# Kernel tuning notes

Hardware: AMD Instinct MI355X
Metric: run time of the kernel (lower is better)

## Reference

```python
import jax, jax.numpy as jnp
import numpy as np

N, LMAX, D, VOCAB, CVOCAB = 50000, 12, 512, 1552, 80


def setup_inputs() -> dict:
    key = jax.random.key(0)
    ks = jax.random.split(key, 8)
    return {
        "word_ids": jax.random.randint(ks[0], (N,), 0, VOCAB),
        "char_ids": jax.random.randint(ks[1], (N, LMAX), 0, CVOCAB),
        "char_lens": jax.random.randint(ks[2], (N,), 1, LMAX + 1),
        "word_embed_table": jax.random.normal(ks[3], (VOCAB, D), jnp.float32) * 0.02,
        "char_embed_table": jax.random.normal(ks[4], (CVOCAB, D), jnp.float32) * 0.02,
        "char_proj_w": jax.random.normal(ks[5], (D,), jnp.float32) * 0.04,
        "char_proj_b": jnp.zeros((1,), jnp.float32),
        "word_proj_w": jax.random.normal(ks[6], (D,), jnp.float32) * 0.04,
        "word_proj_b": jnp.zeros((1,), jnp.float32),
        "clf_w": jax.random.normal(ks[7], (VOCAB, D), jnp.float32) * 0.04,
        "clf_b": jnp.zeros((VOCAB,), jnp.float32),
    }


def reference(word_ids, char_ids, char_lens, word_embed_table, char_embed_table,
              char_proj_w, char_proj_b, word_proj_w, word_proj_b, clf_w, clf_b):
    # word embedding lookup: [N, D]
    we = word_embed_table[word_ids]
    # char embedding lookup (padded): [N, L, D]
    ce = char_embed_table[char_ids]
    # char_proj = Linear(512, 1): scores per char, [N, L]
    pre = jnp.einsum("nld,d->nl", ce, char_proj_w) + char_proj_b
    # mask out padding (reproduces the ragged per-word loop of the original)
    mask = (jnp.arange(LMAX) < char_lens[:, None]).astype(pre.dtype)  # [N, L]
    # attn_weights = pre_attn^T @ word_char_embed per word -> [N, D]
    char_pool = jnp.einsum("nl,nld->nd", pre * mask, ce)
    # all_embed = sigmoid(word_embed * char_embed): [N, D]
    all_embed = jax.nn.sigmoid(we * char_pool)
    # word_proj = Linear(512, 1) + Swish(beta=1): [N]
    wa = jnp.einsum("nd,d->n", all_embed, word_proj_w) + word_proj_b
    wa = wa * jax.nn.sigmoid(wa)
    # word_weights = word_attn^T @ all_embed: [1, D]
    word_weights = jnp.einsum("n,nd->d", wa, all_embed)[None, :]
    # classifier Linear(512, 1552): [1, VOCAB]
    res = word_weights @ clf_w.T + clf_b
    return (all_embed, res)
```

## Files before the change

kernel.cpp:

```cpp
#include <hip/hip_runtime.h>
#include <math.h>

#define LMAXC 12
#define DIM   512
#define VOC   1552
#define NCHAR 80

typedef float vf4 __attribute__((ext_vector_type(4)));
typedef _Float16 hf8 __attribute__((ext_vector_type(8)));
typedef unsigned short ushort_t;

#define WW8_OFF 0
#define U_OFF   4096
#define WT_OFF  25600

__device__ __forceinline__ float sigmoidf_fast(float x) {
    return 1.0f / (1.0f + __expf(-x));
}

__device__ __forceinline__ ushort_t f2bf(float f) {
    unsigned u = __float_as_uint(f);
    u = (u + 0x7fffu + ((u >> 16) & 1u)) >> 16;
    return (ushort_t)u;
}

__global__ __launch_bounds__(256)
void setup_kernel(const float* __restrict__ ctab,
                  const float* __restrict__ cpw,
                  const float* __restrict__ cpb,
                  const float* __restrict__ wtab,
                  float*       __restrict__ ws)
{
    __shared__ float red[4];
    const int b   = blockIdx.x;
    const int tid = threadIdx.x;
    _Float16* uh = (_Float16*)(ws + U_OFF);

    if (b < NCHAR) {
        const float a0 = ctab[b * DIM + tid];
        const float a1 = ctab[b * DIM + tid + 256];
        float p = a0 * cpw[tid] + a1 * cpw[tid + 256];
        #pragma unroll
        for (int off = 32; off > 0; off >>= 1) p += __shfl_xor(p, off, 64);
        if ((tid & 63) == 0) red[tid >> 6] = p;
        __syncthreads();
        const float s = red[0] + red[1] + red[2] + red[3] + cpb[0];
        uh[b * DIM + tid]       = (_Float16)(s * a0);
        uh[b * DIM + tid + 256] = (_Float16)(s * a1);
    } else if (b == NCHAR) {
        for (int i = tid; i < 8 * DIM; i += 256) ws[WW8_OFF + i] = 0.f;
        uh[NCHAR * DIM + tid]       = (_Float16)0.f;
        uh[NCHAR * DIM + tid + 256] = (_Float16)0.f;
    } else {
        const int r0 = (b - NCHAR - 1) * 4;
        ushort_t* wt16 = (ushort_t*)(ws + WT_OFF);
        #pragma unroll
        for (int i = 0; i < 8; ++i) {
            const int idx = r0 * DIM + i * 256 + tid;
            wt16[idx] = f2bf(wtab[idx]);
        }
    }
}

__device__ __forceinline__ void bf8_unpack(uint4 v, float* f) {
    f[0] = __uint_as_float(v.x << 16); f[1] = __uint_as_float(v.x & 0xffff0000u);
    f[2] = __uint_as_float(v.y << 16); f[3] = __uint_as_float(v.y & 0xffff0000u);
    f[4] = __uint_as_float(v.z << 16); f[5] = __uint_as_float(v.z & 0xffff0000u);
    f[6] = __uint_as_float(v.w << 16); f[7] = __uint_as_float(v.w & 0xffff0000u);
}

__global__ __launch_bounds__(256)
void fused_word_kernel(const int*   __restrict__ word_ids,
                       const int*   __restrict__ char_ids,
                       const int*   __restrict__ char_lens,
                       const float* __restrict__ wpw,
                       const float* __restrict__ wpb,
                       const float* __restrict__ ws,
                       float*       __restrict__ all_embed,
                       float*       __restrict__ ww8,
                       int n)
{
    const int lane = threadIdx.x & 63;
    const int wv   = threadIdx.x >> 6;
    const int d0   = lane << 3;
    const _Float16* uh   = (const _Float16*)(ws + U_OFF);
    const ushort_t* wt16 = (const ushort_t*)(ws + WT_OFF);

    const vf4 pw0 = *(const vf4*)(wpw + d0);
    const vf4 pw1 = *(const vf4*)(wpw + d0 + 4);
    const float wb = wpb[0];

    vf4 acc0 = {0.f, 0.f, 0.f, 0.f};
    vf4 acc1 = {0.f, 0.f, 0.f, 0.f};

    const int gw0     = (blockIdx.x << 2) + wv;
    const int gstride = gridDim.x << 2;

    int wu = 0, wid = 0, len = 0;
    int4 ci0 = {0,0,0,0}, ci1 = ci0, ci2 = ci0;

    int w = gw0;
    if (w < n) {
        wu  = __builtin_amdgcn_readfirstlane(w);
        wid = word_ids[wu];
        len = char_lens[wu];
        const int4* cp = (const int4*)(char_ids + (size_t)wu * LMAXC);
        ci0 = cp[0]; ci1 = cp[1]; ci2 = cp[2];
    }

    while (w < n) {
        const int wn  = w + gstride;
        const int wun = __builtin_amdgcn_readfirstlane(wn < n ? wn : 0);
        const int widn = word_ids[wun];
        const int lenn = char_lens[wun];
        const int4* cpn = (const int4*)(char_ids + (size_t)wun * LMAXC);
        const int4 m0 = cpn[0], m1 = cpn[1], m2 = cpn[2];

        const uint4 wvec = *(const uint4*)(wt16 + (size_t)wid * DIM + d0);

        const int cid[LMAXC] = {ci0.x, ci0.y, ci0.z, ci0.w,
                                ci1.x, ci1.y, ci1.z, ci1.w,
                                ci2.x, ci2.y, ci2.z, ci2.w};
        int cide[LMAXC];
        #pragma unroll
        for (int l = 0; l < LMAXC; ++l) cide[l] = (l < len) ? cid[l] : NCHAR;

        hf8 hsA = (hf8)(_Float16)0.f;
        hf8 hsB = (hf8)(_Float16)0.f;
        #pragma unroll
        for (int l = 0; l < LMAXC; l += 2) {
            const hf8 rA = *(const hf8*)(uh + cide[l]     * DIM + d0);
            const hf8 rB = *(const hf8*)(uh + cide[l + 1] * DIM + d0);
            hsA += rA;
            hsB += rB;
        }
        const hf8 hs = hsA + hsB;

        float p[8];
        #pragma unroll
        for (int j = 0; j < 8; ++j) p[j] = (float)hs[j];

        float we[8];
        bf8_unpack(wvec, we);
        float ae[8];
        #pragma unroll
        for (int j = 0; j < 8; ++j) ae[j] = sigmoidf_fast(we[j] * p[j]);

        const vf4 a0v = {ae[0], ae[1], ae[2], ae[3]};
        const vf4 a1v = {ae[4], ae[5], ae[6], ae[7]};

        float* op = all_embed + (size_t)wu * DIM + d0;
        __builtin_nontemporal_store(a0v, (vf4*)op);
        __builtin_nontemporal_store(a1v, (vf4*)(op + 4));

        float s = ae[0]*pw0.x + ae[1]*pw0.y + ae[2]*pw0.z + ae[3]*pw0.w
                + ae[4]*pw1.x + ae[5]*pw1.y + ae[6]*pw1.z + ae[7]*pw1.w;
        #pragma unroll
        for (int off = 32; off > 0; off >>= 1)
            s += __shfl_xor(s, off, 64);
        float wa = s + wb;
        wa = wa * sigmoidf_fast(wa);

        acc0 += wa * a0v;
        acc1 += wa * a1v;

        w = wn; wu = wun; wid = widn; len = lenn;
        ci0 = m0; ci1 = m1; ci2 = m2;
    }

    __shared__ float lds[4][DIM];
    *(vf4*)&lds[wv][d0]     = acc0;
    *(vf4*)&lds[wv][d0 + 4] = acc1;
    __syncthreads();

    const int slice = blockIdx.x & 7;
    for (int d = threadIdx.x; d < DIM; d += 256) {
        const float s = lds[0][d] + lds[1][d] + lds[2][d] + lds[3][d];
        atomicAdd(ww8 + slice * DIM + d, s);
    }
}

__global__ __launch_bounds__(256)
void clf_kernel(const float* __restrict__ ww8,
                const float* __restrict__ clf_w,
                const float* __restrict__ clf_b,
                float*       __restrict__ res)
{
    const int lane = threadIdx.x & 63;
    const int wv   = threadIdx.x >> 6;
    const int v    = (blockIdx.x << 2) + wv;
    if (v >= VOC) return;

    const int d0 = lane << 3;
    float w[8];
    #pragma unroll
    for (int j = 0; j < 8; ++j) w[j] = 0.f;
    #pragma unroll
    for (int s = 0; s < 8; ++s) {
        const float4 a = *(const float4*)(ww8 + s * DIM + d0);
        const float4 b = *(const float4*)(ww8 + s * DIM + d0 + 4);
        w[0] += a.x; w[1] += a.y; w[2] += a.z; w[3] += a.w;
        w[4] += b.x; w[5] += b.y; w[6] += b.z; w[7] += b.w;
    }

    const float* cr = clf_w + (size_t)v * DIM + d0;
    const float4 a0 = *(const float4*)(cr);
    const float4 a1 = *(const float4*)(cr + 4);
    float p = w[0]*a0.x + w[1]*a0.y + w[2]*a0.z + w[3]*a0.w
            + w[4]*a1.x + w[5]*a1.y + w[6]*a1.z + w[7]*a1.w;
    #pragma unroll
    for (int off = 32; off > 0; off >>= 1)
        p += __shfl_xor(p, off, 64);
    if (lane == 0) res[v] = p + clf_b[v];
}

extern "C" void kernel_launch(void* const* d_in, const int* in_sizes, int n_in,
                              void* d_out, int out_size, void* d_ws, size_t ws_size,
                              hipStream_t stream) {
    const int*   word_ids  = (const int*)  d_in[0];
    const int*   char_ids  = (const int*)  d_in[1];
    const int*   char_lens = (const int*)  d_in[2];
    const float* wtab      = (const float*)d_in[3];
    const float* ctab      = (const float*)d_in[4];
    const float* cpw       = (const float*)d_in[5];
    const float* cpb       = (const float*)d_in[6];
    const float* wpw       = (const float*)d_in[7];
    const float* wpb       = (const float*)d_in[8];
    const float* clf_w     = (const float*)d_in[9];
    const float* clf_b     = (const float*)d_in[10];

    const int n = in_sizes[0];
    float* out       = (float*)d_out;
    float* all_embed = out;
    float* res       = out + (size_t)n * DIM;
    float* ws        = (float*)d_ws;

    setup_kernel<<<NCHAR + 1 + (VOC / 4), 256, 0, stream>>>(ctab, cpw, cpb, wtab, ws);

    fused_word_kernel<<<2048, 256, 0, stream>>>(
        word_ids, char_ids, char_lens,
        wpw, wpb, ws, all_embed, ws + WW8_OFF, n);

    clf_kernel<<<(VOC + 3) / 4, 256, 0, stream>>>(ws + WW8_OFF, clf_w, clf_b, res);
}
```

Before: 47.08 us.

## Store scaled char table as FP8, stage it in LDS, prefetch word rows

The precomputed scaled char-embedding table is stored as FP8 with a power-of-two scale, which the word table absorbs as an inverse scale. Each block copies the whole table (about 41 KB) into LDS, so the gathers read shared memory instead of global or L2. The word-table row for the next word is now prefetched one iteration ahead, and blocks grow to 512 threads with half as many blocks. FP8 quantisation lowers accuracy of the char pooling, and the per-block LDS fill plus higher LDS use may reduce occupancy.

```diff
diff --git a/kernel.cpp b/kernel.cpp
--- a/kernel.cpp
+++ b/kernel.cpp
@@ -5,14 +5,17 @@
 #define DIM   512
 #define VOC   1552
 #define NCHAR 80
+#define SCALE     4096.0f
+#define INV_SCALE (1.0f/4096.0f)
 
 typedef float vf4 __attribute__((ext_vector_type(4)));
-typedef _Float16 hf8 __attribute__((ext_vector_type(8)));
+typedef float vf2 __attribute__((ext_vector_type(2)));
 typedef unsigned short ushort_t;
 
 #define WW8_OFF 0
 #define U_OFF   4096
-#define WT_OFF  25600
+#define U_BYTE_OFF 16384
+#define WT_OFF  14464
 
 __device__ __forceinline__ float sigmoidf_fast(float x) {
     return 1.0f / (1.0f + __expf(-x));
@@ -22,6 +25,41 @@
     unsigned u = __float_as_uint(f);
     u = (u + 0x7fffu + ((u >> 16) & 1u)) >> 16;
     return (ushort_t)u;
+}
+
+#if __has_builtin(__builtin_amdgcn_cvt_pk_fp8_f32) && __has_builtin(__builtin_amdgcn_cvt_pk_f32_fp8)
+#define HW_FP8 1
+#else
+#define HW_FP8 0
+#endif
+
+#if !HW_FP8
+__device__ __forceinline__ unsigned char f2fp8_sw(float f) {
+    unsigned u = __float_as_uint(f);
+    unsigned s = (u >> 24) & 0x80u;
+    float a = fabsf(f);
+    if (a < 0.015625f) return (unsigned char)s;
+    if (a > 448.f) a = 448.f;
+    u = __float_as_uint(a);
+    u = u + 0x7ffffu + ((u >> 20) & 1u);
+    int e8 = (int)(u >> 23) - 120;
+    if (e8 <= 0) return (unsigned char)s;
+    if (e8 > 15) e8 = 15;
+    return (unsigned char)(s | (e8 << 3) | ((u >> 20) & 7u));
+}
+__device__ __forceinline__ float fp8_to_f32_sw(unsigned b) {
+    unsigned e = (b >> 3) & 15u, m = b & 7u, s = (b & 0x80u) << 24;
+    if (e == 0) return __uint_as_float(s);
+    return __uint_as_float(s | ((e + 120u) << 23) | (m << 20));
+}
+#endif
+
+__device__ __forceinline__ ushort_t pack2_fp8(float f0, float f1) {
+#if HW_FP8
+    return (ushort_t)(__builtin_amdgcn_cvt_pk_fp8_f32(f0, f1, 0, false) & 0xffffu);
+#else
+    return (ushort_t)(f2fp8_sw(f0) | ((unsigned)f2fp8_sw(f1) << 8));
+#endif
 }
 
 __global__ __launch_bounds__(256)
@@ -34,30 +72,28 @@
     __shared__ float red[4];
     const int b   = blockIdx.x;
     const int tid = threadIdx.x;
-    _Float16* uh = (_Float16*)(ws + U_OFF);
+    unsigned char* u8 = (unsigned char*)ws + U_BYTE_OFF;
 
     if (b < NCHAR) {
-        const float a0 = ctab[b * DIM + tid];
-        const float a1 = ctab[b * DIM + tid + 256];
-        float p = a0 * cpw[tid] + a1 * cpw[tid + 256];
+        const float a0 = ctab[b * DIM + 2 * tid];
+        const float a1 = ctab[b * DIM + 2 * tid + 1];
+        float p = a0 * cpw[2 * tid] + a1 * cpw[2 * tid + 1];
         #pragma unroll
         for (int off = 32; off > 0; off >>= 1) p += __shfl_xor(p, off, 64);
         if ((tid & 63) == 0) red[tid >> 6] = p;
         __syncthreads();
-        const float s = red[0] + red[1] + red[2] + red[3] + cpb[0];
-        uh[b * DIM + tid]       = (_Float16)(s * a0);
-        uh[b * DIM + tid + 256] = (_Float16)(s * a1);
+        const float s = (red[0] + red[1] + red[2] + red[3] + cpb[0]) * SCALE;
+        ((ushort_t*)u8)[b * 256 + tid] = pack2_fp8(s * a0, s * a1);
     } else if (b == NCHAR) {
         for (int i = tid; i < 8 * DIM; i += 256) ws[WW8_OFF + i] = 0.f;
-        uh[NCHAR * DIM + tid]       = (_Float16)0.f;
-        uh[NCHAR * DIM + tid + 256] = (_Float16)0.f;
+        if (tid < 128) ((unsigned int*)(u8 + NCHAR * DIM))[tid] = 0u;
     } else {
         const int r0 = (b - NCHAR - 1) * 4;
         ushort_t* wt16 = (ushort_t*)(ws + WT_OFF);
         #pragma unroll
         for (int i = 0; i < 8; ++i) {
             const int idx = r0 * DIM + i * 256 + tid;
-            wt16[idx] = f2bf(wtab[idx]);
+            wt16[idx] = f2bf(wtab[idx] * INV_SCALE);
         }
     }
 }
@@ -69,7 +105,7 @@
     f[6] = __uint_as_float(v.w << 16); f[7] = __uint_as_float(v.w & 0xffff0000u);
 }
 
-__global__ __launch_bounds__(256)
+__global__ __launch_bounds__(512)
 void fused_word_kernel(const int*   __restrict__ word_ids,
                        const int*   __restrict__ char_ids,
                        const int*   __restrict__ char_lens,
@@ -80,10 +116,18 @@
                        float*       __restrict__ ww8,
                        int n)
 {
+    __shared__ __align__(16) unsigned char smem[41472];
+
+    {
+        const uint4* src = (const uint4*)((const unsigned char*)ws + U_BYTE_OFF);
+        uint4* dst = (uint4*)smem;
+        for (int i = threadIdx.x; i < 2592; i += 512) dst[i] = src[i];
+    }
+    __syncthreads();
+
     const int lane = threadIdx.x & 63;
     const int wv   = threadIdx.x >> 6;
     const int d0   = lane << 3;
-    const _Float16* uh   = (const _Float16*)(ws + U_OFF);
     const ushort_t* wt16 = (const ushort_t*)(ws + WT_OFF);
 
     const vf4 pw0 = *(const vf4*)(wpw + d0);
@@ -93,30 +137,31 @@
     vf4 acc0 = {0.f, 0.f, 0.f, 0.f};
     vf4 acc1 = {0.f, 0.f, 0.f, 0.f};
 
-    const int gw0     = (blockIdx.x << 2) + wv;
-    const int gstride = gridDim.x << 2;
-
-    int wu = 0, wid = 0, len = 0;
+    const int gw0     = (blockIdx.x << 3) + wv;
+    const int gstride = gridDim.x << 3;
+
+    int wu = 0, len = 0;
     int4 ci0 = {0,0,0,0}, ci1 = ci0, ci2 = ci0;
+    uint4 wvec = {0,0,0,0};
 
     int w = gw0;
     if (w < n) {
         wu  = __builtin_amdgcn_readfirstlane(w);
-        wid = word_ids[wu];
+        const int wid = word_ids[wu];
         len = char_lens[wu];
         const int4* cp = (const int4*)(char_ids + (size_t)wu * LMAXC);
         ci0 = cp[0]; ci1 = cp[1]; ci2 = cp[2];
+        wvec = *(const uint4*)(wt16 + (size_t)wid * DIM + d0);
     }
 
     while (w < n) {
-        const int wn  = w + gstride;
-        const int wun = __builtin_amdgcn_readfirstlane(wn < n ? wn : 0);
+        const int wn   = w + gstride;
+        const int wun  = __builtin_amdgcn_readfirstlane(wn < n ? wn : 0);
         const int widn = word_ids[wun];
         const int lenn = char_lens[wun];
         const int4* cpn = (const int4*)(char_ids + (size_t)wun * LMAXC);
         const int4 m0 = cpn[0], m1 = cpn[1], m2 = cpn[2];
-
-        const uint4 wvec = *(const uint4*)(wt16 + (size_t)wid * DIM + d0);
+        const uint4 wvecn = *(const uint4*)(wt16 + (size_t)widn * DIM + d0);
 
         const int cid[LMAXC] = {ci0.x, ci0.y, ci0.z, ci0.w,
                                 ci1.x, ci1.y, ci1.z, ci1.w,
@@ -125,20 +170,23 @@
         #pragma unroll
         for (int l = 0; l < LMAXC; ++l) cide[l] = (l < len) ? cid[l] : NCHAR;
 
-        hf8 hsA = (hf8)(_Float16)0.f;
-        hf8 hsB = (hf8)(_Float16)0.f;
-        #pragma unroll
-        for (int l = 0; l < LMAXC; l += 2) {
-            const hf8 rA = *(const hf8*)(uh + cide[l]     * DIM + d0);
-            const hf8 rB = *(const hf8*)(uh + cide[l + 1] * DIM + d0);
-            hsA += rA;
-            hsB += rB;
+        vf2 q0 = {0.f, 0.f}, q1 = q0, q2 = q0, q3 = q0;
+        #pragma unroll
+        for (int l = 0; l < LMAXC; ++l) {
+            const uint2 rv = *(const uint2*)(smem + cide[l] * DIM + (lane << 3));
+#if HW_FP8
+            q0 += __builtin_amdgcn_cvt_pk_f32_fp8((int)rv.x, false);
+            q1 += __builtin_amdgcn_cvt_pk_f32_fp8((int)rv.x, true);
+            q2 += __builtin_amdgcn_cvt_pk_f32_fp8((int)rv.y, false);
+            q3 += __builtin_amdgcn_cvt_pk_f32_fp8((int)rv.y, true);
+#else
+            q0.x += fp8_to_f32_sw(rv.x & 0xffu);        q0.y += fp8_to_f32_sw((rv.x >> 8) & 0xffu);
+            q1.x += fp8_to_f32_sw((rv.x >> 16) & 0xffu); q1.y += fp8_to_f32_sw(rv.x >> 24);
+            q2.x += fp8_to_f32_sw(rv.y & 0xffu);        q2.y += fp8_to_f32_sw((rv.y >> 8) & 0xffu);
+            q3.x += fp8_to_f32_sw((rv.y >> 16) & 0xffu); q3.y += fp8_to_f32_sw(rv.y >> 24);
+#endif
         }
-        const hf8 hs = hsA + hsB;
-
-        float p[8];
-        #pragma unroll
-        for (int j = 0; j < 8; ++j) p[j] = (float)hs[j];
+        const float p[8] = {q0.x, q0.y, q1.x, q1.y, q2.x, q2.y, q3.x, q3.y};
 
         float we[8];
         bf8_unpack(wvec, we);
@@ -164,18 +212,21 @@
         acc0 += wa * a0v;
         acc1 += wa * a1v;
 
-        w = wn; wu = wun; wid = widn; len = lenn;
-        ci0 = m0; ci1 = m1; ci2 = m2;
-    }
-
-    __shared__ float lds[4][DIM];
-    *(vf4*)&lds[wv][d0]     = acc0;
-    *(vf4*)&lds[wv][d0 + 4] = acc1;
+        w = wn; wu = wun; len = lenn;
+        ci0 = m0; ci1 = m1; ci2 = m2; wvec = wvecn;
+    }
+
     __syncthreads();
+    float* red = (float*)smem;
+    *(vf4*)(red + wv * DIM + d0)     = acc0;
+    *(vf4*)(red + wv * DIM + d0 + 4) = acc1;
+    __syncthreads();
 
     const int slice = blockIdx.x & 7;
-    for (int d = threadIdx.x; d < DIM; d += 256) {
-        const float s = lds[0][d] + lds[1][d] + lds[2][d] + lds[3][d];
+    for (int d = threadIdx.x; d < DIM; d += 512) {
+        float s = 0.f;
+        #pragma unroll
+        for (int k = 0; k < 8; ++k) s += red[k * DIM + d];
         atomicAdd(ww8 + slice * DIM + d, s);
     }
 }
@@ -237,7 +288,7 @@
 
     setup_kernel<<<NCHAR + 1 + (VOC / 4), 256, 0, stream>>>(ctab, cpw, cpb, wtab, ws);
 
-    fused_word_kernel<<<2048, 256, 0, stream>>>(
+    fused_word_kernel<<<1024, 512, 0, stream>>>(
         word_ids, char_ids, char_lens,
         wpw, wpb, ws, all_embed, ws + WW8_OFF, n);
 
```

New measurement: 44.89 us. 4.7% less time.
